# Performance work log

Measured on AMD Instinct MI355X. Metric: run time of the kernel, lower is better.

## Reference

```python
import jax, jax.numpy as jnp
import numpy as np

DIM = 128      # embedding dim (c)
HEAD_DIM = 32
NH = DIM // HEAD_DIM          # 4 mLSTM heads
INNER = 256                    # round_up(2*DIM, 64)
DH = INNER // NH               # 64 per-head dim
K = 4                          # causal conv kernel size
BS = 4                         # qkv_proj_blocksize
NB = INNER // BS               # 64 block-diagonal qkv blocks
B, T, H, W = 8, 16, 32, 32


def setup_inputs() -> dict:
    key = jax.random.key(0)
    ks = jax.random.split(key, 12)
    s = 0.02
    return {
        "x": jax.random.normal(ks[0], (B, DIM, T, H, W), jnp.float32),
        "W_up": jax.random.normal(ks[1], (DIM, 2 * INNER), jnp.float32) * s,
        "conv_w": jax.random.normal(ks[2], (K, 1, INNER), jnp.float32) * s,  # depthwise causal conv (WIO)
        "conv_b": jnp.zeros((INNER,), jnp.float32),
        "Wq": jax.random.normal(ks[3], (NB, BS, BS), jnp.float32) * s,  # block-diag headwise linear
        "Wk": jax.random.normal(ks[4], (NB, BS, BS), jnp.float32) * s,
        "Wv": jax.random.normal(ks[5], (NB, BS, BS), jnp.float32) * s,
        "ig_w": jax.random.normal(ks[6], (3 * INNER, NH), jnp.float32) * s,
        "ig_b": jnp.zeros((NH,), jnp.float32),
        "fg_w": jax.random.normal(ks[7], (3 * INNER, NH), jnp.float32) * s,
        "fg_b": jnp.zeros((NH,), jnp.float32),
        "ln_w": jnp.ones((INNER,), jnp.float32),   # multi-head layernorm scale
        "skip": jnp.ones((INNER,), jnp.float32),   # learnable skip
        "W_down": jax.random.normal(ks[8], (INNER, DIM), jnp.float32) * s,
    }


def _headwise(y, Wh):
    # block-diagonal linear: y [B,S,INNER] split into NB blocks of BS
    Bx, S, _ = y.shape
    yb = y.reshape(Bx, S, NB, BS)
    return jnp.einsum('bsni,noi->bsno', yb, Wh).reshape(Bx, S, INNER)


def _mlstm_parallel(q, k, v, ig, fg):
    # q,k,v: [B,NH,S,DH]; ig,fg (gate preacts): [B,NH,S]
    S = q.shape[2]
    log_f = jax.nn.log_sigmoid(fg)
    lf_cum = jnp.concatenate(
        [jnp.zeros_like(log_f[..., :1]), jnp.cumsum(log_f, axis=-1)], axis=-1)  # [B,NH,S+1]
    logfg = lf_cum[..., 1:, None] - lf_cum[..., None, 1:]                      # [B,NH,S,S]
    mask = jnp.tril(jnp.ones((S, S), bool))
    logfg = jnp.where(mask, logfg, -jnp.inf)
    log_D = logfg + ig[..., None, :]
    max_log_D = jnp.max(log_D, axis=-1, keepdims=True)
    Dmat = jnp.exp(log_D - max_log_D)
    qk = jnp.einsum('bhsd,bhtd->bhst', q, k) / jnp.sqrt(jnp.float32(q.shape[-1]))
    C = qk * Dmat
    normalizer = jnp.maximum(jnp.abs(C.sum(-1, keepdims=True)), jnp.exp(-max_log_D))
    return jnp.einsum('bhst,bhtd->bhsd', C / (normalizer + 1e-6), v)


def _forward(x, W_up, conv_w, conv_b, Wq, Wk, Wv, ig_w, ig_b, fg_w, fg_b, ln_w, skip, W_down):
    b, c, t, hh, ww = x.shape
    xs = jnp.transpose(x, (0, 3, 4, 2, 1)).reshape(b * hh * ww, t, c)  # (b h w) t c
    up = xs @ W_up
    x_m, z = jnp.split(up, 2, axis=-1)                                  # [Bx,S,INNER] each
    # depthwise causal conv + swish
    xc = jax.lax.conv_general_dilated(
        x_m, conv_w, (1,), [(K - 1, 0)],
        dimension_numbers=('NWC', 'WIO', 'NWC'), feature_group_count=INNER) + conv_b
    xc = jax.nn.silu(xc)
    q = _headwise(xc, Wq)
    k = _headwise(xc, Wk)
    v = _headwise(x_m, Wv)
    if_in = jnp.concatenate([q, k, v], axis=-1)
    ig = if_in @ ig_w + ig_b                                            # [Bx,S,NH]
    fg = if_in @ fg_w + fg_b
    Bx, S = q.shape[0], q.shape[1]
    qh = q.reshape(Bx, S, NH, DH).transpose(0, 2, 1, 3)
    kh = k.reshape(Bx, S, NH, DH).transpose(0, 2, 1, 3)
    vh = v.reshape(Bx, S, NH, DH).transpose(0, 2, 1, 3)
    ht = _mlstm_parallel(qh, kh, vh, ig.transpose(0, 2, 1), fg.transpose(0, 2, 1))  # [Bx,NH,S,DH]
    # multi-head (group) layernorm over DH, weight only
    mu = ht.mean(-1, keepdims=True)
    var = ht.var(-1, keepdims=True)
    hn = (ht - mu) / jnp.sqrt(var + 1e-5) * ln_w.reshape(NH, DH)[None, :, None, :]
    hn = hn.transpose(0, 2, 1, 3).reshape(Bx, S, INNER)
    h_state = (hn + skip * xc) * jax.nn.silu(z)
    out = h_state @ W_down                                              # [Bx,S,DIM]
    return out.reshape(b, hh, ww, t, c).transpose(0, 4, 3, 1, 2)        # b c t h w


def reference(x, W_up, conv_w, conv_b, Wq, Wk, Wv, ig_w, ig_b, fg_w, fg_b, ln_w, skip, W_down):
    return _forward(x, W_up, conv_w, conv_b, Wq, Wk, Wv, ig_w, ig_b, fg_w, fg_b, ln_w, skip, W_down)
```

## Files before the change

### kernel.cpp

```cpp
#include <hip/hip_runtime.h>
#include <cmath>


typedef __attribute__((ext_vector_type(8))) short short8;
typedef __attribute__((ext_vector_type(4))) short short4v;
typedef __attribute__((ext_vector_type(4))) float f32x4;
typedef unsigned short ushort_t;

static __device__ __forceinline__ float siluf(float v) {
  return v / (1.0f + __expf(-v));
}
static __device__ __forceinline__ float logsigf(float v) {
  return fminf(v, 0.f) - log1pf(__expf(-fabsf(v)));
}
static __device__ __forceinline__ float sel4(float4 w, int idx) {
  float r = w.x;
  r = (idx == 1) ? w.y : r;
  r = (idx == 2) ? w.z : r;
  r = (idx == 3) ? w.w : r;
  return r;
}
static __device__ __forceinline__ ushort_t f2bf(float x) {
  unsigned u = __float_as_uint(x);
  return (ushort_t)((u + 0x7fffu + ((u >> 16) & 1u)) >> 16);
}
static __device__ __forceinline__ float bf2f(ushort_t h) {
  return __uint_as_float(((unsigned)h) << 16);
}

__global__ __launch_bounds__(256)
void prep_w(const float* __restrict__ Wup, const float* __restrict__ Wd,
            const float* __restrict__ igw, const float* __restrict__ fgw,
            ushort_t* __restrict__ wt_hi, ushort_t* __restrict__ wt_lo,
            ushort_t* __restrict__ wdt_hi, ushort_t* __restrict__ wdt_lo,
            ushort_t* __restrict__ wgf)
{
  const int g = blockIdx.x * 256 + threadIdx.x;
  if (g < 65536) {
    const int c = g >> 9, j = g & 511;
    const float w = Wup[g];
    const ushort_t h = f2bf(w);
    wt_hi[j*128 + c] = h;
    wt_lo[j*128 + c] = f2bf(w - bf2f(h));
  } else if (g < 98304) {
    const int g2 = g - 65536;
    const int j = g2 >> 7, c = g2 & 127;
    const float w = Wd[g2];
    const ushort_t h = f2bf(w);
    wdt_hi[c*256 + j] = h;
    wdt_lo[c*256 + j] = f2bf(w - bf2f(h));
  } else if (g < 110592) {
    const int e = g - 98304;
    const int kc = e >> 9;
    const int lane = (e >> 3) & 63;
    const int i = e & 7;
    const int n = lane & 15;
    const int kq = kc*32 + (lane >> 4)*8 + i;
    float val = 0.f;
    if (n < 4)      val = igw[kq*4 + n];
    else if (n < 8) val = fgw[kq*4 + (n - 4)];
    wgf[e] = f2bf(val);
  }
}

#define AS 72

__global__ __launch_bounds__(256, 3)
void up_gemm(const float* __restrict__ x,
             const ushort_t* __restrict__ wt_hi, const ushort_t* __restrict__ wt_lo,
             ushort_t* __restrict__ xmb, ushort_t* __restrict__ szb)
{
  __shared__ ushort_t sAhi[128*AS];
  __shared__ ushort_t sAlo[128*AS];

  const int tid = threadIdx.x;
  const int hw0 = blockIdx.x * 128;
  const int j0  = blockIdx.y * 128;
  const int bt  = blockIdx.z;
  const int b   = bt >> 4, t = bt & 15;

  const int wv = tid >> 6;
  const int wm = wv >> 1, wn = wv & 1;
  const int ln = tid & 63;
  const int lm = ln & 15;
  const int q  = ln >> 4;

  const int hwL = tid & 127;
  const int cg  = tid >> 7;

  f32x4 acc[4][4];
  #pragma unroll
  for (int i = 0; i < 4; ++i)
    #pragma unroll
    for (int k = 0; k < 4; ++k) acc[i][k] = (f32x4){0.f, 0.f, 0.f, 0.f};

  for (int stage = 0; stage < 2; ++stage) {
    #pragma unroll
    for (int p = 0; p < 8; ++p) {
      const int cl = p*8 + cg*4;
      const int c  = stage*64 + cl;
      const float* xp = &x[((b*128 + c)*16 + t)*1024 + hw0 + hwL];
      const float v0 = xp[0], v1 = xp[16384], v2 = xp[32768], v3 = xp[49152];
      const ushort_t h0 = f2bf(v0), h1 = f2bf(v1), h2 = f2bf(v2), h3 = f2bf(v3);
      const ushort_t l0 = f2bf(v0 - bf2f(h0)), l1 = f2bf(v1 - bf2f(h1));
      const ushort_t l2 = f2bf(v2 - bf2f(h2)), l3 = f2bf(v3 - bf2f(h3));
      *(ushort4*)&sAhi[hwL*AS + cl] = make_ushort4(h0, h1, h2, h3);
      *(ushort4*)&sAlo[hwL*AS + cl] = make_ushort4(l0, l1, l2, l3);
    }
    __syncthreads();

    #pragma unroll
    for (int s = 0; s < 2; ++s) {
      const int kc = s*32 + q*8;
      const int kg = stage*64 + kc;
      short8 bh[4], bl[4];
      #pragma unroll
      for (int nt = 0; nt < 4; ++nt) {
        const int jr = j0 + wn*64 + nt*16 + lm;
        bh[nt] = *(const short8*)&wt_hi[jr*128 + kg];
        bl[nt] = *(const short8*)&wt_lo[jr*128 + kg];
      }
      #pragma unroll
      for (int mt = 0; mt < 4; ++mt) {
        const int ao = (wm*64 + mt*16 + lm)*AS + kc;
        const short8 ah = *(const short8*)&sAhi[ao];
        const short8 al = *(const short8*)&sAlo[ao];
        #pragma unroll
        for (int nt = 0; nt < 4; ++nt) {
          acc[mt][nt] = __builtin_amdgcn_mfma_f32_16x16x32_bf16(ah, bh[nt], acc[mt][nt], 0, 0, 0);
          acc[mt][nt] = __builtin_amdgcn_mfma_f32_16x16x32_bf16(ah, bl[nt], acc[mt][nt], 0, 0, 0);
          acc[mt][nt] = __builtin_amdgcn_mfma_f32_16x16x32_bf16(al, bh[nt], acc[mt][nt], 0, 0, 0);
        }
      }
    }
    __syncthreads();
  }

  const bool isz = (j0 >= 256);
  #pragma unroll
  for (int mt = 0; mt < 4; ++mt) {
    #pragma unroll
    for (int nt = 0; nt < 4; ++nt) {
      const int jc = j0 + wn*64 + nt*16 + lm;
      #pragma unroll
      for (int r = 0; r < 4; ++r) {
        const int rowg = bt*1024 + hw0 + wm*64 + mt*16 + q*4 + r;
        const float v = acc[mt][nt][r];
        if (!isz) xmb[rowg*256 + jc] = f2bf(v);
        else      szb[rowg*256 + (jc - 256)] = f2bf(siluf(v));
      }
    }
  }
}

#define SQ 264
#define SXC 260

__global__ __launch_bounds__(256, 4)
void seq_kernel(const ushort_t* __restrict__ xm_ws,
                ushort_t* szh,
                const float* __restrict__ conv_w, const float* __restrict__ conv_b,
                const float* __restrict__ Wq, const float* __restrict__ Wk,
                const float* __restrict__ Wv,
                const ushort_t* __restrict__ wgf,
                const float* __restrict__ igb, const float* __restrict__ fgb,
                const float* __restrict__ lnw, const float* __restrict__ skipw)
{
  __shared__ __align__(16) ushort_t q_lds[16*SQ];
  __shared__ __align__(16) ushort_t k_lds[16*SQ];
  __shared__ __align__(16) ushort_t v_lds[16*SQ];
  __shared__ __align__(16) ushort_t xc_lds[16*SXC];
  __shared__ __align__(16) ushort_t p_lds[4*16*36];
  __shared__ __align__(16) float s_gpart[512];
  __shared__ float s_ig[64];
  __shared__ float s_lf[64];

  const int tid = threadIdx.x;
  const int j   = tid;
  const int l2  = j & 3;
  const int seq = blockIdx.x;
  const int rbase = (seq >> 10) * 16384 + (seq & 1023);

  const int w    = tid >> 6;
  const int ln   = tid & 63;
  const int g    = ln >> 4;
  const int lc   = ln & 15;
  const int hb2  = w * 64;

  const float4 wq4 = *(const float4*)&Wq[j*4];
  const float4 wk4 = *(const float4*)&Wk[j*4];
  const float4 wv4 = *(const float4*)&Wv[j*4];
  float wqp[4], wkp[4], wvp[4];
  #pragma unroll
  for (int d = 0; d < 4; ++d) {
    const int idx = l2 ^ d;
    wqp[d] = sel4(wq4, idx);
    wkp[d] = sel4(wk4, idx);
    wvp[d] = sel4(wv4, idx);
  }
  const float cw0 = conv_w[j],     cw1 = conv_w[256+j];
  const float cw2 = conv_w[512+j], cw3 = conv_w[768+j];
  const float cb  = conv_b[j];

  float p1 = 0.f, p2 = 0.f, p3 = 0.f;
  #pragma unroll
  for (int t = 0; t < 16; ++t) {
    const float m = bf2f(xm_ws[(rbase + t*1024)*256 + j]);
    const float pre = cw0*p3 + cw1*p2 + cw2*p1 + cw3*m + cb;
    const float x = siluf(pre);
    p3 = p2; p2 = p1; p1 = m;
    const float x1 = __shfl_xor(x, 1), x2 = __shfl_xor(x, 2), x3 = __shfl_xor(x, 3);
    const float m1 = __shfl_xor(m, 1), m2 = __shfl_xor(m, 2), m3 = __shfl_xor(m, 3);
    const float qv = x*wqp[0] + x1*wqp[1] + x2*wqp[2] + x3*wqp[3];
    const float kv = x*wkp[0] + x1*wkp[1] + x2*wkp[2] + x3*wkp[3];
    const float vv = m*wvp[0] + m1*wvp[1] + m2*wvp[2] + m3*wvp[3];
    q_lds [t*SQ  + j] = f2bf(qv);
    k_lds [t*SQ  + j] = f2bf(kv);
    v_lds [t*SQ  + j] = f2bf(vv);
    xc_lds[t*SXC + j] = f2bf(x);
  }
  __syncthreads();

  f32x4 gacc = (f32x4){0.f, 0.f, 0.f, 0.f};
  #pragma unroll
  for (int c6 = 0; c6 < 6; ++c6) {
    const int kc = w*6 + c6;
    const ushort_t* yb = (kc < 8) ? q_lds : (kc < 16) ? k_lds : v_lds;
    const int klocal = (kc & 7)*32;
    const short8 ya = *(const short8*)&yb[lc*SQ + klocal + g*8];
    const short8 wb = *(const short8*)&wgf[(kc*64 + ln)*8];
    gacc = __builtin_amdgcn_mfma_f32_16x16x32_bf16(ya, wb, gacc, 0, 0, 0);
  }
  f32x4 qkacc = (f32x4){0.f, 0.f, 0.f, 0.f};
  {
    const short8 qa0 = *(const short8*)&q_lds[lc*SQ + hb2 + g*8];
    const short8 qa1 = *(const short8*)&q_lds[lc*SQ + hb2 + 32 + g*8];
    const short8 kb0 = *(const short8*)&k_lds[lc*SQ + hb2 + g*8];
    const short8 kb1 = *(const short8*)&k_lds[lc*SQ + hb2 + 32 + g*8];
    qkacc = __builtin_amdgcn_mfma_f32_16x16x32_bf16(qa0, kb0, qkacc, 0, 0, 0);
    qkacc = __builtin_amdgcn_mfma_f32_16x16x32_bf16(qa1, kb1, qkacc, 0, 0, 0);
  }
  if (lc < 8) {
    #pragma unroll
    for (int r = 0; r < 4; ++r)
      s_gpart[w*128 + (g*4 + r)*8 + lc] = gacc[r];
  }
  __syncthreads();

  if (tid < 128) {
    const int t = tid >> 3, n = tid & 7;
    const float s = s_gpart[t*8+n] + s_gpart[128 + t*8+n]
                  + s_gpart[256 + t*8+n] + s_gpart[384 + t*8+n];
    if (n < 4) s_ig[t*4 + n] = s + igb[n];
    else       s_lf[t*4 + (n-4)] = logsigf(s + fgb[n-4]);
  }
  __syncthreads();

  float* s_lfc = s_gpart;
  if (tid < 4) {
    float run = 0.f;
    s_lfc[tid] = 0.f;
    #pragma unroll
    for (int t = 0; t < 16; ++t) { run += s_lf[t*4 + tid]; s_lfc[(t+1)*4 + tid] = run; }
  }
  __syncthreads();

  {
    const int tcol = lc;
    const float lfc_t1 = s_lfc[(tcol+1)*4 + w];
    const float igt    = s_ig[tcol*4 + w];
    float ld[4], mloc[4];
    #pragma unroll
    for (int r = 0; r < 4; ++r) {
      const int s = g*4 + r;
      const float lfs = s_lfc[(s+1)*4 + w];
      ld[r] = (tcol <= s) ? (lfs - lfc_t1 + igt) : -INFINITY;
      mloc[r] = ld[r];
    }
    #pragma unroll
    for (int off = 1; off < 16; off <<= 1) {
      #pragma unroll
      for (int r = 0; r < 4; ++r) mloc[r] = fmaxf(mloc[r], __shfl_xor(mloc[r], off));
    }
    float cs[4], rsum[4];
    #pragma unroll
    for (int r = 0; r < 4; ++r) {
      const int s = g*4 + r;
      cs[r] = (tcol <= s) ? (qkacc[r] * 0.125f) * __expf(ld[r] - mloc[r]) : 0.f;
      rsum[r] = cs[r];
    }
    #pragma unroll
    for (int off = 1; off < 16; off <<= 1) {
      #pragma unroll
      for (int r = 0; r < 4; ++r) rsum[r] += __shfl_xor(rsum[r], off);
    }
    #pragma unroll
    for (int r = 0; r < 4; ++r) {
      const float denom = fmaxf(fabsf(rsum[r]), __expf(-mloc[r])) + 1e-6f;
      const float pv = cs[r] / denom;
      p_lds[(w*16 + g*4 + r)*36 + tcol] = f2bf(pv);
    }
  }
  __syncthreads();

  f32x4 oacc[4];
  #pragma unroll
  for (int c = 0; c < 4; ++c) oacc[c] = (f32x4){0.f, 0.f, 0.f, 0.f};
  {
    const int tb = g*8;
    short8 pa = (short8){0,0,0,0,0,0,0,0};
    if (tb < 16) {
      const short4v plo = *(const short4v*)&p_lds[(w*16 + lc)*36 + tb];
      const short4v phi = *(const short4v*)&p_lds[(w*16 + lc)*36 + tb + 4];
      pa[0]=plo[0]; pa[1]=plo[1]; pa[2]=plo[2]; pa[3]=plo[3];
      pa[4]=phi[0]; pa[5]=phi[1]; pa[6]=phi[2]; pa[7]=phi[3];
    }
    #pragma unroll
    for (int c = 0; c < 4; ++c) {
      short8 vb;
      #pragma unroll
      for (int i = 0; i < 8; ++i)
        vb[i] = (short)v_lds[((tb + i) & 15)*SQ + hb2 + c*16 + lc];
      oacc[c] = __builtin_amdgcn_mfma_f32_16x16x32_bf16(pa, vb, oacc[c], 0, 0, 0);
    }
  }

  float lnc[4], skc[4];
  #pragma unroll
  for (int c = 0; c < 4; ++c) {
    const int ch = hb2 + c*16 + lc;
    lnc[c] = lnw[ch];
    skc[c] = skipw[ch];
  }
  #pragma unroll
  for (int r = 0; r < 4; ++r) {
    const int s = g*4 + r;
    float tot = oacc[0][r] + oacc[1][r] + oacc[2][r] + oacc[3][r];
    #pragma unroll
    for (int off = 1; off < 16; off <<= 1) tot += __shfl_xor(tot, off);
    const float mu = tot * (1.f/64.f);
    float var = 0.f;
    #pragma unroll
    for (int c = 0; c < 4; ++c) { const float d = oacc[c][r] - mu; var += d*d; }
    #pragma unroll
    for (int off = 1; off < 16; off <<= 1) var += __shfl_xor(var, off);
    const float rstd = rsqrtf(var * (1.f/64.f) + 1e-5f);
    #pragma unroll
    for (int c = 0; c < 4; ++c) {
      const int ch = hb2 + c*16 + lc;
      const float hn = (oacc[c][r] - mu) * rstd * lnc[c];
      const float xcv = bf2f(xc_lds[s*SXC + ch]);
      const long long off_g = (long long)(rbase + s*1024)*256 + ch;
      const float szv = bf2f(szh[off_g]);
      szh[off_g] = f2bf((hn + skc[c]*xcv) * szv);
    }
  }
}

__global__ __launch_bounds__(256, 3)
void down_gemm(const ushort_t* __restrict__ hb,
               const ushort_t* __restrict__ wdt_hi, const ushort_t* __restrict__ wdt_lo,
               float* __restrict__ out)
{
  const int tid = threadIdx.x;
  const int hw0 = blockIdx.x * 128;
  const int bt  = blockIdx.z;
  const int bq  = bt >> 4, tq = bt & 15;
  const int rowbase = bt*1024 + hw0;

  const int wv = tid >> 6;
  const int wm = wv >> 1, wn = wv & 1;
  const int ln = tid & 63;
  const int lm = ln & 15;
  const int q  = ln >> 4;

  f32x4 acc[4][4];
  #pragma unroll
  for (int i = 0; i < 4; ++i)
    #pragma unroll
    for (int k = 0; k < 4; ++k) acc[i][k] = (f32x4){0.f, 0.f, 0.f, 0.f};

  #pragma unroll 2
  for (int kc = 0; kc < 256; kc += 32) {
    const int kq = kc + q*8;
    short8 ah[4], al[4];
    #pragma unroll
    for (int mt = 0; mt < 4; ++mt) {
      const int c = wm*64 + mt*16 + lm;
      ah[mt] = *(const short8*)&wdt_hi[c*256 + kq];
      al[mt] = *(const short8*)&wdt_lo[c*256 + kq];
    }
    #pragma unroll
    for (int nt = 0; nt < 4; ++nt) {
      const int n = wn*64 + nt*16 + lm;
      const short8 bf = *(const short8*)&hb[(rowbase + n)*256 + kq];
      #pragma unroll
      for (int mt = 0; mt < 4; ++mt) {
        acc[mt][nt] = __builtin_amdgcn_mfma_f32_16x16x32_bf16(ah[mt], bf, acc[mt][nt], 0, 0, 0);
        acc[mt][nt] = __builtin_amdgcn_mfma_f32_16x16x32_bf16(al[mt], bf, acc[mt][nt], 0, 0, 0);
      }
    }
  }

  #pragma unroll
  for (int mt = 0; mt < 4; ++mt) {
    #pragma unroll
    for (int nt = 0; nt < 4; ++nt) {
      const int hw = hw0 + wn*64 + nt*16 + lm;
      #pragma unroll
      for (int r = 0; r < 4; ++r) {
        const int c = wm*64 + mt*16 + q*4 + r;
        out[((bq*128 + c)*16 + tq)*1024 + hw] = acc[mt][nt][r];
      }
    }
  }
}

extern "C" void kernel_launch(void* const* d_in, const int* in_sizes, int n_in,
                              void* d_out, int out_size, void* d_ws, size_t ws_size,
                              hipStream_t stream)
{
  const float* x      = (const float*)d_in[0];
  const float* Wup    = (const float*)d_in[1];
  const float* conv_w = (const float*)d_in[2];
  const float* conv_b = (const float*)d_in[3];
  const float* Wq     = (const float*)d_in[4];
  const float* Wk     = (const float*)d_in[5];
  const float* Wv     = (const float*)d_in[6];
  const float* igw    = (const float*)d_in[7];
  const float* igb    = (const float*)d_in[8];
  const float* fgw    = (const float*)d_in[9];
  const float* fgb    = (const float*)d_in[10];
  const float* lnw    = (const float*)d_in[11];
  const float* skipw  = (const float*)d_in[12];
  const float* Wd     = (const float*)d_in[13];
  float* out = (float*)d_out;

  ushort_t* xmb    = (ushort_t*)d_ws;
  ushort_t* szb    = xmb + 33554432;
  ushort_t* wt_hi  = (ushort_t*)((char*)d_ws + 134217728);
  ushort_t* wt_lo  = wt_hi + 65536;
  ushort_t* wdt_hi = wt_lo + 65536;
  ushort_t* wdt_lo = wdt_hi + 32768;
  ushort_t* wgf    = wdt_lo + 32768;

  prep_w<<<432, 256, 0, stream>>>(Wup, Wd, igw, fgw,
                                  wt_hi, wt_lo, wdt_hi, wdt_lo, wgf);
  up_gemm<<<dim3(8, 4, 128), 256, 0, stream>>>(x, wt_hi, wt_lo, xmb, szb);
  seq_kernel<<<8192, 256, 0, stream>>>(xmb, szb,
                                       conv_w, conv_b, Wq, Wk, Wv,
                                       wgf, igb, fgb, lnw, skipw);
  down_gemm<<<dim3(8, 1, 128), 256, 0, stream>>>(szb, wdt_hi, wdt_lo, out);
}
```

Before: 391.9 us.

## Pre-split x into bf16 hi/lo, pre-swizzle weights, stage GEMM epilogue through LDS

Adds a prep_x kernel that transposes x into row-major bf16 hi/lo buffers, so up_gemm loads A tiles with 16-byte vector reads instead of strided fp32 gathers and per-tile conversion. The weights are pre-packed into MFMA fragment order so each lane reads a contiguous short8. The up_gemm epilogue now goes through LDS to issue coalesced 16-byte stores. The cost is an extra kernel and a 64MB round trip to write and re-read the split x, and up_gemm's occupancy hint rises to 4.

```diff
diff --git a/kernel.cpp b/kernel.cpp
--- a/kernel.cpp
+++ b/kernel.cpp
@@ -29,28 +29,62 @@
 }
 
 __global__ __launch_bounds__(256)
+void prep_x(const float* __restrict__ x,
+            ushort_t* __restrict__ xt_hi, ushort_t* __restrict__ xt_lo)
+{
+  const int hw = blockIdx.x * 256 + threadIdx.x;
+  const int bt = blockIdx.y;
+  const int b  = bt >> 4, t = bt & 15;
+  const int row = bt * 1024 + hw;
+  const float* xb = &x[(b*128*16 + t)*1024 + hw];
+
+  #pragma unroll
+  for (int c0 = 0; c0 < 128; c0 += 8) {
+    short8 hv, lv;
+    #pragma unroll
+    for (int ii = 0; ii < 8; ++ii) {
+      const float v = xb[(c0 + ii) * 16384];
+      const ushort_t h = f2bf(v);
+      hv[ii] = (short)h;
+      lv[ii] = (short)f2bf(v - bf2f(h));
+    }
+    *(short8*)&xt_hi[row*128 + c0] = hv;
+    *(short8*)&xt_lo[row*128 + c0] = lv;
+  }
+}
+
+__global__ __launch_bounds__(256)
 void prep_w(const float* __restrict__ Wup, const float* __restrict__ Wd,
             const float* __restrict__ igw, const float* __restrict__ fgw,
-            ushort_t* __restrict__ wt_hi, ushort_t* __restrict__ wt_lo,
-            ushort_t* __restrict__ wdt_hi, ushort_t* __restrict__ wdt_lo,
+            ushort_t* __restrict__ wtf, ushort_t* __restrict__ wdtf,
             ushort_t* __restrict__ wgf)
 {
   const int g = blockIdx.x * 256 + threadIdx.x;
-  if (g < 65536) {
-    const int c = g >> 9, j = g & 511;
-    const float w = Wup[g];
+  if (g < 131072) {
+    const int i   = g & 7;
+    const int ln  = (g >> 3) & 63;
+    const int hl  = (g >> 9) & 1;
+    const int kc  = (g >> 10) & 3;
+    const int j16 = g >> 12;
+    const int c = kc*32 + (ln >> 4)*8 + i;
+    const int j = j16*16 + (ln & 15);
+    const float w = Wup[c*512 + j];
     const ushort_t h = f2bf(w);
-    wt_hi[j*128 + c] = h;
-    wt_lo[j*128 + c] = f2bf(w - bf2f(h));
-  } else if (g < 98304) {
-    const int g2 = g - 65536;
-    const int j = g2 >> 7, c = g2 & 127;
-    const float w = Wd[g2];
+    wtf[g] = hl ? f2bf(w - bf2f(h)) : h;
+  } else if (g < 196608) {
+    const int e   = g - 131072;
+    const int i   = e & 7;
+    const int ln  = (e >> 3) & 63;
+    const int hl  = (e >> 9) & 1;
+    const int kc  = (e >> 10) & 7;
+    const int c16 = e >> 13;
+    const int m = c16*16 + (ln & 15);
+    const int k = kc*32 + (ln >> 4)*8 + i;
+    const float w = Wd[k*128 + m];
     const ushort_t h = f2bf(w);
-    wdt_hi[c*256 + j] = h;
-    wdt_lo[c*256 + j] = f2bf(w - bf2f(h));
-  } else if (g < 110592) {
-    const int e = g - 98304;
+    wdtf[e] = hl ? f2bf(w - bf2f(h)) : h;
+  } else if (g < 208896) {
+    const int e = g - 196608;
     const int kc = e >> 9;
     const int lane = (e >> 3) & 63;
     const int i = e & 7;
@@ -63,21 +97,20 @@
   }
 }
 
-#define AS 72
-
-__global__ __launch_bounds__(256, 3)
-void up_gemm(const float* __restrict__ x,
-             const ushort_t* __restrict__ wt_hi, const ushort_t* __restrict__ wt_lo,
+__global__ __launch_bounds__(256, 4)
+void up_gemm(const ushort_t* __restrict__ xt_hi, const ushort_t* __restrict__ xt_lo,
+             const ushort_t* __restrict__ wtf,
              ushort_t* __restrict__ xmb, ushort_t* __restrict__ szb)
 {
-  __shared__ ushort_t sAhi[128*AS];
-  __shared__ ushort_t sAlo[128*AS];
+  __shared__ __align__(16) ushort_t ldsbuf[2*128*72];
+  ushort_t* sAhi = ldsbuf;
+  ushort_t* sAlo = ldsbuf + 128*72;
 
   const int tid = threadIdx.x;
   const int hw0 = blockIdx.x * 128;
   const int j0  = blockIdx.y * 128;
   const int bt  = blockIdx.z;
-  const int b   = bt >> 4, t = bt & 15;
+  const int rowbase = bt*1024 + hw0;
 
   const int wv = tid >> 6;
   const int wm = wv >> 1, wn = wv & 1;
@@ -85,9 +118,6 @@
   const int lm = ln & 15;
   const int q  = ln >> 4;
 
-  const int hwL = tid & 127;
-  const int cg  = tid >> 7;
-
   f32x4 acc[4][4];
   #pragma unroll
   for (int i = 0; i < 4; ++i)
@@ -96,33 +126,32 @@
 
   for (int stage = 0; stage < 2; ++stage) {
     #pragma unroll
-    for (int p = 0; p < 8; ++p) {
-      const int cl = p*8 + cg*4;
-      const int c  = stage*64 + cl;
-      const float* xp = &x[((b*128 + c)*16 + t)*1024 + hw0 + hwL];
-      const float v0 = xp[0], v1 = xp[16384], v2 = xp[32768], v3 = xp[49152];
-      const ushort_t h0 = f2bf(v0), h1 = f2bf(v1), h2 = f2bf(v2), h3 = f2bf(v3);
-      const ushort_t l0 = f2bf(v0 - bf2f(h0)), l1 = f2bf(v1 - bf2f(h1));
-      const ushort_t l2 = f2bf(v2 - bf2f(h2)), l3 = f2bf(v3 - bf2f(h3));
-      *(ushort4*)&sAhi[hwL*AS + cl] = make_ushort4(h0, h1, h2, h3);
-      *(ushort4*)&sAlo[hwL*AS + cl] = make_ushort4(l0, l1, l2, l3);
+    for (int p = 0; p < 4; ++p) {
+      const int row = wv*32 + p*8 + (ln >> 3);
+      const int ck  = (ln & 7) * 8;
+      const int gidx = (rowbase + row)*128 + stage*64 + ck;
+      const short8 hv = *(const short8*)&xt_hi[gidx];
+      const short8 lv = *(const short8*)&xt_lo[gidx];
+      *(short8*)&sAhi[row*72 + ck] = hv;
+      *(short8*)&sAlo[row*72 + ck] = lv;
     }
     __syncthreads();
 
     #pragma unroll
     for (int s = 0; s < 2; ++s) {
-      const int kc = s*32 + q*8;
-      const int kg = stage*64 + kc;
+      const int kc = stage*2 + s;
       short8 bh[4], bl[4];
       #pragma unroll
       for (int nt = 0; nt < 4; ++nt) {
-        const int jr = j0 + wn*64 + nt*16 + lm;
-        bh[nt] = *(const short8*)&wt_hi[jr*128 + kg];
-        bl[nt] = *(const short8*)&wt_lo[jr*128 + kg];
+        const int j16 = (j0 >> 4) + wn*4 + nt;
+        const int base = (j16*4 + kc)*1024;
+        bh[nt] = *(const short8*)&wtf[base + ln*8];
+        bl[nt] = *(const short8*)&wtf[base + 512 + ln*8];
       }
+      const int ck = (s*4 + q)*8;
       #pragma unroll
       for (int mt = 0; mt < 4; ++mt) {
-        const int ao = (wm*64 + mt*16 + lm)*AS + kc;
+        const int ao = (wm*64 + mt*16 + lm)*72 + ck;
         const short8 ah = *(const short8*)&sAhi[ao];
         const short8 al = *(const short8*)&sAlo[ao];
         #pragma unroll
@@ -137,18 +166,31 @@
   }
 
   const bool isz = (j0 >= 256);
+  ushort_t* eL = ldsbuf;
   #pragma unroll
   for (int mt = 0; mt < 4; ++mt) {
     #pragma unroll
     for (int nt = 0; nt < 4; ++nt) {
-      const int jc = j0 + wn*64 + nt*16 + lm;
+      const int col = wn*64 + nt*16 + lm;
       #pragma unroll
       for (int r = 0; r < 4; ++r) {
-        const int rowg = bt*1024 + hw0 + wm*64 + mt*16 + q*4 + r;
-        const float v = acc[mt][nt][r];
-        if (!isz) xmb[rowg*256 + jc] = f2bf(v);
-        else      szb[rowg*256 + (jc - 256)] = f2bf(siluf(v));
+        const int row = wm*64 + mt*16 + q*4 + r;
+        float v = acc[mt][nt][r];
+        if (isz) v = siluf(v);
+        eL[row*136 + col] = f2bf(v);
       }
+    }
+  }
+  __syncthreads();
+  {
+    const int rq = ln >> 4, ck = ln & 15;
+    #pragma unroll
+    for (int p = 0; p < 8; ++p) {
+      const int row = wv*32 + p*4 + rq;
+      const short8 val = *(const short8*)&eL[row*136 + ck*8];
+      const int rowg = rowbase + row;
+      if (!isz) *(short8*)&xmb[rowg*256 + j0 + ck*8] = val;
+      else      *(short8*)&szb[rowg*256 + (j0 - 256) + ck*8] = val;
     }
   }
 }
@@ -359,7 +401,7 @@
 
 __global__ __launch_bounds__(256, 3)
 void down_gemm(const ushort_t* __restrict__ hb,
-               const ushort_t* __restrict__ wdt_hi, const ushort_t* __restrict__ wdt_lo,
+               const ushort_t* __restrict__ wdtf,
                float* __restrict__ out)
 {
   const int tid = threadIdx.x;
@@ -383,12 +425,13 @@
   #pragma unroll 2
   for (int kc = 0; kc < 256; kc += 32) {
     const int kq = kc + q*8;
+    const int kcIdx = kc >> 5;
     short8 ah[4], al[4];
     #pragma unroll
     for (int mt = 0; mt < 4; ++mt) {
-      const int c = wm*64 + mt*16 + lm;
-      ah[mt] = *(const short8*)&wdt_hi[c*256 + kq];
-      al[mt] = *(const short8*)&wdt_lo[c*256 + kq];
+      const int base = ((wm*4 + mt)*8 + kcIdx)*1024;
+      ah[mt] = *(const short8*)&wdtf[base + ln*8];
+      al[mt] = *(const short8*)&wdtf[base + 512 + ln*8];
     }
     #pragma unroll
     for (int nt = 0; nt < 4; ++nt) {
@@ -436,19 +479,19 @@
   const float* Wd     = (const float*)d_in[13];
   float* out = (float*)d_out;
 
-  ushort_t* xmb    = (ushort_t*)d_ws;
-  ushort_t* szb    = xmb + 33554432;
-  ushort_t* wt_hi  = (ushort_t*)((char*)d_ws + 134217728);
-  ushort_t* wt_lo  = wt_hi + 65536;
-  ushort_t* wdt_hi = wt_lo + 65536;
-  ushort_t* wdt_lo = wdt_hi + 32768;
-  ushort_t* wgf    = wdt_lo + 32768;
-
-  prep_w<<<432, 256, 0, stream>>>(Wup, Wd, igw, fgw,
-                                  wt_hi, wt_lo, wdt_hi, wdt_lo, wgf);
-  up_gemm<<<dim3(8, 4, 128), 256, 0, stream>>>(x, wt_hi, wt_lo, xmb, szb);
+  ushort_t* xt_hi = (ushort_t*)d_ws;
+  ushort_t* xt_lo = xt_hi + 16777216;
+  ushort_t* xmb   = (ushort_t*)((char*)d_ws + 67108864);
+  ushort_t* szb   = (ushort_t*)((char*)d_ws + 134217728);
+  ushort_t* wtf   = (ushort_t*)((char*)d_ws + 201326592);
+  ushort_t* wdtf  = wtf + 131072;
+  ushort_t* wgf   = wdtf + 65536;
+
+  prep_x<<<dim3(4, 128), 256, 0, stream>>>(x, xt_hi, xt_lo);
+  prep_w<<<816, 256, 0, stream>>>(Wup, Wd, igw, fgw, wtf, wdtf, wgf);
+  up_gemm<<<dim3(8, 4, 128), 256, 0, stream>>>(xt_hi, xt_lo, wtf, xmb, szb);
   seq_kernel<<<8192, 256, 0, stream>>>(xmb, szb,
                                        conv_w, conv_b, Wq, Wk, Wv,
                                        wgf, igb, fgb, lnw, skipw);
-  down_gemm<<<dim3(8, 1, 128), 256, 0, stream>>>(szb, wdt_hi, wdt_lo, out);
-}
+  down_gemm<<<dim3(8, 1, 128), 256, 0, stream>>>(szb, wdtf, out);
+}
```

Result: no change. 397.4 us (+1.4%).
